# Kernel optimization log

Hardware: AMD Instinct MI355X
Metric: run time of the kernel (lower is better)

Reference implementation:

```python
import jax, jax.numpy as jnp
import numpy as np

N_HEAD = 8
EPS_LN = 1e-5
EPS_SM = 1e-16


def _mlp(x, w1, b1, g, beta, w2, b2):
    # Linear -> ReLU -> LayerNorm -> Linear (matches nn.Sequential in torch module)
    h = jax.nn.relu(x @ w1 + b1)
    mu = jnp.mean(h, axis=-1, keepdims=True)
    var = jnp.mean((h - mu) ** 2, axis=-1, keepdims=True)
    h = (h - mu) * jax.lax.rsqrt(var + EPS_LN) * g + beta
    return h @ w2 + b2


def setup_inputs() -> dict:
    B, L, D, E, Fe, H = 4, 4096, 128, 262144, 5, N_HEAD
    ks = jax.random.split(jax.random.key(0), 20)
    s = 0.02
    p = lambda i, sh: jax.random.normal(ks[i], sh, jnp.float32) * s
    z = lambda n: jnp.zeros((n,), jnp.float32)
    inp = {
        "key": jax.random.normal(ks[0], (B, L, D), jnp.float32),
        "value": jax.random.normal(ks[1], (B, L, D), jnp.float32),
        "query": jax.random.normal(ks[2], (B, L, D), jnp.float32),
        "edge_feats": jax.random.normal(ks[3], (E, Fe), jnp.float32),
        "atten_masks": jnp.zeros((E,), jnp.float32),  # present in signature, unused in forward
        "batch_indices": jax.random.randint(ks[4], (E,), 0, B),
        "head_indices": jax.random.randint(ks[5], (E,), 0, L),
        "tail_indices": jax.random.randint(ks[6], (E,), 0, L),
        "key_w": p(7, (D, D)), "key_b": z(D),
        "query_w": p(8, (D, D)), "query_b": z(D),
        "value_w": p(9, (D, D)), "value_b": z(D),
        "proj_w": p(10, (D, D)), "proj_b": z(D),
        "ea_w1": p(11, (Fe, D)), "ea_b1": z(D), "ea_g": jnp.ones((D,), jnp.float32), "ea_beta": z(D), "ea_w2": p(12, (D, H)), "ea_b2": z(H),
        "ek_w1": p(13, (Fe, D)), "ek_b1": z(D), "ek_g": jnp.ones((D,), jnp.float32), "ek_beta": z(D), "ek_w2": p(14, (D, D)), "ek_b2": z(D),
        "ev_w1": p(15, (Fe, D)), "ev_b1": z(D), "ev_g": jnp.ones((D,), jnp.float32), "ev_beta": z(D), "ev_w2": p(16, (D, D)), "ev_b2": z(D),
    }
    return inp


def reference(key, value, query, edge_feats, atten_masks,
              batch_indices, head_indices, tail_indices,
              key_w, key_b, query_w, query_b, value_w, value_b, proj_w, proj_b,
              ea_w1, ea_b1, ea_g, ea_beta, ea_w2, ea_b2,
              ek_w1, ek_b1, ek_g, ek_beta, ek_w2, ek_b2,
              ev_w1, ev_b1, ev_g, ev_beta, ev_w2, ev_b2):
    B, L, D = query.shape
    H = N_HEAD
    dh = D // H
    N = B * L
    # node projections -> [B*L, H, dh]
    k = (key @ key_w + key_b).reshape(N, H, dh)
    q = (query @ query_w + query_b).reshape(N, H, dh)
    v = (value @ value_w + value_b).reshape(N, H, dh)
    heads = batch_indices * L + head_indices  # destination node per edge
    tails = batch_indices * L + tail_indices  # source node per edge
    # per-edge gather + edge-conditioned k/v
    qs = q[heads]
    ks = k[tails] + _mlp(edge_feats, ek_w1, ek_b1, ek_g, ek_beta, ek_w2, ek_b2).reshape(-1, H, dh)
    vs = v[tails] + _mlp(edge_feats, ev_w1, ev_b1, ev_g, ev_beta, ev_w2, ev_b2).reshape(-1, H, dh)
    w = jnp.sum(ks * qs, axis=-1) + _mlp(edge_feats, ea_w1, ea_b1, ea_g, ea_beta, ea_w2, ea_b2)  # [E, H]
    # segment softmax over edges grouped by destination node
    m = jax.ops.segment_max(w, heads, num_segments=N)
    ex = jnp.exp(w - m[heads])
    denom = jax.ops.segment_sum(ex, heads, num_segments=N)
    att = ex / (denom[heads] + EPS_SM)  # [E, H]
    # weighted scatter-sum combine
    y = jax.ops.segment_sum(att[:, :, None] * vs, heads, num_segments=N).reshape(B, L, D)
    return y @ proj_w + proj_b
```

## Files before the change

kernel.cpp:

```cpp
#include <hip/hip_runtime.h>
#include <hip/hip_bf16.h>

#define D      128
#define NHEAD  8
#define FE     5
#define LSEQ   4096
#define EPB    64
#define NNODE  16384
#define EPS_LN 1e-5f
#define EPS_SM 1e-16f

typedef unsigned short ushort_t;
typedef __bf16 bf16x8 __attribute__((ext_vector_type(8)));
typedef float  f32x4  __attribute__((ext_vector_type(4)));

__device__ __forceinline__ ushort_t f2bf(float x) {
    __hip_bfloat16 b = __float2bfloat16(x);
    return __builtin_bit_cast(unsigned short, b);
}
__device__ __forceinline__ float bf2f(ushort_t u) {
    __hip_bfloat16 b = __builtin_bit_cast(__hip_bfloat16, u);
    return __bfloat162float(b);
}
__device__ __forceinline__ float i2f(int x)  { return __builtin_bit_cast(float, x); }
__device__ __forceinline__ int   f2i(float x){ return __builtin_bit_cast(int, x); }

union Pk8 { ushort_t u[8]; uint4 v; };

__global__ __launch_bounds__(256) void pre_kernel(
    const float* __restrict__ ekw2, const float* __restrict__ evw2,
    const float* __restrict__ eaw2,
    const float* __restrict__ kw, const float* __restrict__ qw,
    const float* __restrict__ vw,
    ushort_t* __restrict__ eksw, ushort_t* __restrict__ evsw, ushort_t* __restrict__ easw,
    ushort_t* __restrict__ kwsw, ushort_t* __restrict__ qwsw, ushort_t* __restrict__ vwsw,
    const int* __restrict__ bidx, const int* __restrict__ hidx,
    int* __restrict__ cnt, int E)
{
    const int t = threadIdx.x;
    if (blockIdx.x < 41) {
        const int g = blockIdx.x * 256 + t;
        const float* src; ushort_t* dst; int frag, ncols = 128, nvalid = 128;
        if (g < 2048)       { src = ekw2; dst = eksw; frag = g; }
        else if (g < 4096)  { src = evw2; dst = evsw; frag = g - 2048; }
        else if (g < 4352)  { src = eaw2; dst = easw; frag = g - 4096; ncols = 8; nvalid = 8; }
        else if (g < 6400)  { src = kw;   dst = kwsw; frag = g - 4352; }
        else if (g < 8448)  { src = qw;   dst = qwsw; frag = g - 6400; }
        else if (g < 10496) { src = vw;   dst = vwsw; frag = g - 8448; }
        else return;
        const int s = (frag >> 6) & 3;
        const int l = frag & 63;
        const int n = ((frag >> 8) << 4) + (l & 15);
        Pk8 pk;
        #pragma unroll
        for (int j = 0; j < 8; ++j) {
            const int k = s * 32 + (l >> 4) * 8 + j;
            const float v = (n < nvalid) ? src[k * ncols + n] : 0.f;
            pk.u[j] = f2bf(v);
        }
        *(uint4*)(dst + (size_t)frag * 8) = pk.v;
        return;
    }
    const int e = (blockIdx.x - 41) * 256 + t;
    if (e < E) atomicAdd(&cnt[bidx[e] * LSEQ + hidx[e]], 1);
}

__global__ __launch_bounds__(1024) void scan16k(
    const int* __restrict__ cnt, int* __restrict__ base)
{
    __shared__ int part[1024];
    const int t = threadIdx.x;
    int v[16], ex[16], s = 0;
    #pragma unroll
    for (int i = 0; i < 16; ++i) v[i] = cnt[t * 16 + i];
    #pragma unroll
    for (int i = 0; i < 16; ++i) { ex[i] = s; s += v[i]; }
    part[t] = s;
    __syncthreads();
    for (int off = 1; off < 1024; off <<= 1) {
        const int x = (t >= off) ? part[t - off] : 0;
        __syncthreads();
        part[t] += x;
        __syncthreads();
    }
    const int boff = (t > 0) ? part[t - 1] : 0;
    #pragma unroll
    for (int i = 0; i < 16; ++i) base[t * 16 + i] = boff + ex[i];
    if (t == 1023) base[NNODE] = boff + s;
}

__global__ __launch_bounds__(256) void mid_kernel(
    const float* __restrict__ key, const float* __restrict__ value,
    const float* __restrict__ query,
    const float* __restrict__ key_b, const float* __restrict__ value_b,
    const float* __restrict__ query_b,
    const ushort_t* __restrict__ kwsw, const ushort_t* __restrict__ vwsw,
    const ushort_t* __restrict__ qwsw,
    ushort_t* __restrict__ k16, ushort_t* __restrict__ v16, ushort_t* __restrict__ q16,
    const int* __restrict__ bidx, const int* __restrict__ hidx, const int* __restrict__ tidx,
    const float* __restrict__ edge_feats,
    const int* __restrict__ base, int* __restrict__ cnt, float* __restrict__ rec,
    int nqm, int E)
{
    const int t  = threadIdx.x;
    const int nq = 3 * nqm;
    if ((int)blockIdx.x < nq) {
        const int which = blockIdx.x / nqm;
        const int blk   = blockIdx.x % nqm;
        const float* X     = (which == 0) ? key   : (which == 1) ? value   : query;
        const float* bias  = (which == 0) ? key_b : (which == 1) ? value_b : query_b;
        const ushort_t* Ww = (which == 0) ? kwsw  : (which == 1) ? vwsw    : qwsw;
        ushort_t* Y        = (which == 0) ? k16   : (which == 1) ? v16     : q16;

        const int mt    = t >> 6;
        const int l     = t & 63;
        const int rbase = blk * 64 + mt * 16;
        const int colb  = l & 15;
        const int row0  = (l >> 4) * 4;
        const int arow  = rbase + colb;
        const int koff  = (l >> 4) * 8;

        bf16x8 afr[4];
        #pragma unroll
        for (int s = 0; s < 4; ++s) {
            const float4 x0 = *(const float4*)&X[(size_t)arow * D + s * 32 + koff];
            const float4 x1 = *(const float4*)&X[(size_t)arow * D + s * 32 + koff + 4];
            Pk8 p8;
            p8.u[0] = f2bf(x0.x); p8.u[1] = f2bf(x0.y);
            p8.u[2] = f2bf(x0.z); p8.u[3] = f2bf(x0.w);
            p8.u[4] = f2bf(x1.x); p8.u[5] = f2bf(x1.y);
            p8.u[6] = f2bf(x1.z); p8.u[7] = f2bf(x1.w);
            afr[s] = __builtin_bit_cast(bf16x8, p8.v);
        }
        #pragma unroll
        for (int nt = 0; nt < 8; ++nt) {
            f32x4 acc = {0.f, 0.f, 0.f, 0.f};
            #pragma unroll
            for (int s = 0; s < 4; ++s) {
                const bf16x8 bfr = *(const bf16x8*)(Ww + (size_t)((nt * 4 + s) * 64 + l) * 8);
                acc = __builtin_amdgcn_mfma_f32_16x16x32_bf16(afr[s], bfr, acc, 0, 0, 0);
            }
            const int col = nt * 16 + colb;
            const float b = bias[col];
            #pragma unroll
            for (int r = 0; r < 4; ++r)
                Y[(size_t)(rbase + row0 + r) * D + col] = f2bf(acc[r] + b);
        }
        return;
    }

    const int e = (blockIdx.x - nq) * 256 + t;
    if (e >= E) return;
    const int bb = bidx[e];
    const int nh = bb * LSEQ + hidx[e];
    const int nt = bb * LSEQ + tidx[e];
    const int slot = atomicSub(&cnt[nh], 1) - 1;
    const int p = base[nh] + slot;
    float ef[FE];
    #pragma unroll
    for (int f = 0; f < FE; ++f) ef[f] = edge_feats[(size_t)e * FE + f];
    *(float4*)&rec[(size_t)p * 8]     = float4{ef[0], ef[1], ef[2], ef[3]};
    *(float4*)&rec[(size_t)p * 8 + 4] = float4{ef[4], i2f(nh), i2f(nt), 0.f};
}

__global__ __launch_bounds__(256, 4) void edge_kernel(
    const float* __restrict__ rec,
    const float* __restrict__ ea_w1, const float* __restrict__ ea_b1,
    const float* __restrict__ ea_g,  const float* __restrict__ ea_be, const float* __restrict__ ea_b2,
    const float* __restrict__ ek_w1, const float* __restrict__ ek_b1,
    const float* __restrict__ ek_g,  const float* __restrict__ ek_be, const float* __restrict__ ek_b2,
    const float* __restrict__ ev_w1, const float* __restrict__ ev_b1,
    const float* __restrict__ ev_g,  const float* __restrict__ ev_be, const float* __restrict__ ev_b2,
    const ushort_t* __restrict__ easw, const ushort_t* __restrict__ eksw, const ushort_t* __restrict__ evsw,
    const ushort_t* __restrict__ k16, const ushort_t* __restrict__ q16, const ushort_t* __restrict__ v16,
    float* __restrict__ ex_ws, ushort_t* __restrict__ vs_ws)
{
    __shared__ float pw1[3][FE * D];
    __shared__ float pb1[3][D], pg[3][D], pbe[3][D];
    __shared__ float pb2k[D], pb2v[D], pb2a[NHEAD];
    __shared__ float ef_s[EPB][FE];
    __shared__ int   eh_s[EPB], et_s[EPB];

    const int t   = threadIdx.x;
    const int e0g = blockIdx.x * EPB;

    for (int i = t; i < FE * D; i += 256) { pw1[0][i] = ea_w1[i]; pw1[1][i] = ek_w1[i]; pw1[2][i] = ev_w1[i]; }
    if (t < D) {
        pb1[0][t] = ea_b1[t]; pb1[1][t] = ek_b1[t]; pb1[2][t] = ev_b1[t];
        pg [0][t] = ea_g [t]; pg [1][t] = ek_g [t]; pg [2][t] = ev_g [t];
        pbe[0][t] = ea_be[t]; pbe[1][t] = ek_be[t]; pbe[2][t] = ev_be[t];
        pb2k[t] = ek_b2[t];   pb2v[t] = ev_b2[t];
        if (t < NHEAD) pb2a[t] = ea_b2[t];
    }
    if (t < 128) {
        const int pl = t >> 1, half = t & 1;
        const float4 v = *(const float4*)&rec[((size_t)e0g + pl) * 8 + half * 4];
        if (half == 0) {
            ef_s[pl][0] = v.x; ef_s[pl][1] = v.y; ef_s[pl][2] = v.z; ef_s[pl][3] = v.w;
        } else {
            ef_s[pl][4] = v.x; eh_s[pl] = f2i(v.y); et_s[pl] = f2i(v.z);
        }
    }
    __syncthreads();

    const int mt   = t >> 6;
    const int l    = t & 63;
    const int qt   = l & 3;
    const int per  = l >> 2;
    const int row0 = (l >> 4) * 4;
    const int colb = l & 15;
    const int src  = 4 * colb + (l >> 4);
    const int bsrc = (l & 48);

    int tn[4], hnn[4];
    #pragma unroll
    for (int r = 0; r < 4; ++r) { tn[r] = et_s[mt*16 + row0 + r]; hnn[r] = eh_s[mt*16 + row0 + r]; }

    float efr[FE];
    #pragma unroll
    for (int f = 0; f < FE; ++f) efr[f] = ef_s[mt*16 + per][f];

    auto first_layer = [&](int m, uint4 pk[4]) {
        const float4* w1v = (const float4*)&pw1[m][0];
        const float4* b1v = (const float4*)&pb1[m][0];
        const float4* gv  = (const float4*)&pg[m][0];
        const float4* bev = (const float4*)&pbe[m][0];
        float4 hv[4][2];
        float s1 = 0.f, s2 = 0.f;
        #pragma unroll
        for (int s = 0; s < 4; ++s) {
            #pragma unroll
            for (int hc = 0; hc < 2; ++hc) {
                const int idx = s * 8 + qt * 2 + hc;
                float4 a = b1v[idx];
                #pragma unroll
                for (int f = 0; f < FE; ++f) {
                    const float sc = efr[f];
                    const float4 w = w1v[f * 32 + idx];
                    a.x = fmaf(sc, w.x, a.x); a.y = fmaf(sc, w.y, a.y);
                    a.z = fmaf(sc, w.z, a.z); a.w = fmaf(sc, w.w, a.w);
                }
                a.x = fmaxf(a.x, 0.f); a.y = fmaxf(a.y, 0.f);
                a.z = fmaxf(a.z, 0.f); a.w = fmaxf(a.w, 0.f);
                hv[s][hc] = a;
                s1 += a.x + a.y + a.z + a.w;
                s2 += a.x*a.x + a.y*a.y + a.z*a.z + a.w*a.w;
            }
        }
        s1 += __shfl_xor(s1, 1); s1 += __shfl_xor(s1, 2);
        s2 += __shfl_xor(s2, 1); s2 += __shfl_xor(s2, 2);
        const float mu = s1 * (1.f / 128.f);
        const float rs = rsqrtf(s2 * (1.f / 128.f) - mu * mu + EPS_LN);
        #pragma unroll
        for (int s = 0; s < 4; ++s) {
            const int idx = s * 8 + qt * 2;
            const float4 x0 = hv[s][0], x1 = hv[s][1];
            const float4 g0 = gv[idx], g1 = gv[idx + 1];
            const float4 b0 = bev[idx], b1 = bev[idx + 1];
            Pk8 p8;
            p8.u[0] = f2bf(fmaf((x0.x - mu) * rs, g0.x, b0.x));
            p8.u[1] = f2bf(fmaf((x0.y - mu) * rs, g0.y, b0.y));
            p8.u[2] = f2bf(fmaf((x0.z - mu) * rs, g0.z, b0.z));
            p8.u[3] = f2bf(fmaf((x0.w - mu) * rs, g0.w, b0.w));
            p8.u[4] = f2bf(fmaf((x1.x - mu) * rs, g1.x, b1.x));
            p8.u[5] = f2bf(fmaf((x1.y - mu) * rs, g1.y, b1.y));
            p8.u[6] = f2bf(fmaf((x1.z - mu) * rs, g1.z, b1.z));
            p8.u[7] = f2bf(fmaf((x1.w - mu) * rs, g1.w, b1.w));
            pk[s] = p8.v;
        }
    };

    auto gather_afr = [&](const uint4 pk[4], bf16x8 afr[4]) {
        #pragma unroll
        for (int s = 0; s < 4; ++s) {
            uint4 w;
            w.x = (unsigned)__shfl((int)pk[s].x, src);
            w.y = (unsigned)__shfl((int)pk[s].y, src);
            w.z = (unsigned)__shfl((int)pk[s].z, src);
            w.w = (unsigned)__shfl((int)pk[s].w, src);
            afr[s] = __builtin_bit_cast(bf16x8, w);
        }
    };

    uint4 pk[4];
    bf16x8 afr[4];

    float eaacc[4];
    first_layer(0, pk);
    gather_afr(pk, afr);
    {
        f32x4 acc = {0.f, 0.f, 0.f, 0.f};
        #pragma unroll
        for (int s = 0; s < 4; ++s) {
            const bf16x8 bfr = *(const bf16x8*)(easw + (size_t)(s * 64 + l) * 8);
            acc = __builtin_amdgcn_mfma_f32_16x16x32_bf16(afr[s], bfr, acc, 0, 0, 0);
        }
        #pragma unroll
        for (int r = 0; r < 4; ++r) eaacc[r] = acc[r];
    }

    first_layer(1, pk);
    gather_afr(pk, afr);
    #pragma unroll
    for (int nt = 0; nt < NHEAD; ++nt) {
        f32x4 acc = {0.f, 0.f, 0.f, 0.f};
        #pragma unroll
        for (int s = 0; s < 4; ++s) {
            const bf16x8 bfr = *(const bf16x8*)(eksw + (size_t)((nt * 4 + s) * 64 + l) * 8);
            acc = __builtin_amdgcn_mfma_f32_16x16x32_bf16(afr[s], bfr, acc, 0, 0, 0);
        }
        const int col = nt * 16 + colb;
        const float b2 = pb2k[col];
        const float ba = pb2a[nt];
        float pr[4];
        #pragma unroll
        for (int r = 0; r < 4; ++r)
            pr[r] = (acc[r] + b2 + bf2f(k16[(size_t)tn[r] * D + col]))
                    * bf2f(q16[(size_t)hnn[r] * D + col]);
        #pragma unroll
        for (int m = 1; m < 16; m <<= 1) {
            #pragma unroll
            for (int r = 0; r < 4; ++r) pr[r] += __shfl_xor(pr[r], m);
        }
        #pragma unroll
        for (int r = 0; r < 4; ++r) {
            const float ea = __shfl(eaacc[r], bsrc | nt);
            const float ex = __expf(pr[r] + ea + ba);
            if (colb == nt)
                ex_ws[(size_t)(e0g + mt*16 + row0 + r) * NHEAD + nt] = ex;
        }
    }

    first_layer(2, pk);
    gather_afr(pk, afr);
    #pragma unroll
    for (int nt = 0; nt < NHEAD; ++nt) {
        f32x4 acc = {0.f, 0.f, 0.f, 0.f};
        #pragma unroll
        for (int s = 0; s < 4; ++s) {
            const bf16x8 bfr = *(const bf16x8*)(evsw + (size_t)((nt * 4 + s) * 64 + l) * 8);
            acc = __builtin_amdgcn_mfma_f32_16x16x32_bf16(afr[s], bfr, acc, 0, 0, 0);
        }
        const int col = nt * 16 + colb;
        const float b2 = pb2v[col];
        #pragma unroll
        for (int r = 0; r < 4; ++r) {
            const float vs = acc[r] + b2 + bf2f(v16[(size_t)tn[r] * D + col]);
            vs_ws[(size_t)(e0g + mt*16 + row0 + r) * D + col] = f2bf(vs);
        }
    }
}

__global__ __launch_bounds__(512) void agg_out(
    const int* __restrict__ base,
    const float* __restrict__ ex_ws, const ushort_t* __restrict__ vs_ws,
    const float* __restrict__ W, const float* __restrict__ bias,
    float* __restrict__ out)
{
    __shared__ float xs[D][20];
    const int t  = threadIdx.x;
    const int rg = t >> 7;
    const int j  = t & 127;
    const int h  = j >> 4;
    const int n0 = blockIdx.x * 16;

    #pragma unroll
    for (int ni = 0; ni < 4; ++ni) {
        const int n  = n0 + rg * 4 + ni;
        const int s0 = base[n], s1 = base[n + 1];
        float acc = 0.f, den = 0.f;
        int p = s0;
        for (; p + 4 <= s1; p += 4) {
            float ex4[4], vs4[4];
            #pragma unroll
            for (int r = 0; r < 4; ++r) {
                ex4[r] = ex_ws[(size_t)(p + r) * NHEAD + h];
                vs4[r] = bf2f(vs_ws[(size_t)(p + r) * D + j]);
            }
            #pragma unroll
            for (int r = 0; r < 4; ++r) {
                den += ex4[r];
                acc = fmaf(ex4[r], vs4[r], acc);
            }
        }
        for (; p < s1; ++p) {
            const float ex = ex_ws[(size_t)p * NHEAD + h];
            den += ex;
            acc = fmaf(ex, bf2f(vs_ws[(size_t)p * D + j]), acc);
        }
        xs[j][rg * 4 + ni] = acc / (den + EPS_SM);
    }
    __syncthreads();

    float acc[4];
    const float b = bias[j];
    #pragma unroll
    for (int r = 0; r < 4; ++r) acc[r] = b;
    #pragma unroll 4
    for (int i = 0; i < D; ++i) {
        const float w = W[i * D + j];
        const float4 y4 = *(const float4*)&xs[i][rg * 4];
        acc[0] = fmaf(y4.x, w, acc[0]); acc[1] = fmaf(y4.y, w, acc[1]);
        acc[2] = fmaf(y4.z, w, acc[2]); acc[3] = fmaf(y4.w, w, acc[3]);
    }
    #pragma unroll
    for (int r = 0; r < 4; ++r)
        out[(size_t)(n0 + rg * 4 + r) * D + j] = acc[r];
}

extern "C" void kernel_launch(void* const* d_in, const int* in_sizes, int n_in,
                              void* d_out, int out_size, void* d_ws, size_t ws_size,
                              hipStream_t stream)
{
    const float* key        = (const float*)d_in[0];
    const float* value      = (const float*)d_in[1];
    const float* query      = (const float*)d_in[2];
    const float* edge_feats = (const float*)d_in[3];
    const int*   bidx       = (const int*)d_in[5];
    const int*   hidx       = (const int*)d_in[6];
    const int*   tidx       = (const int*)d_in[7];
    const float* key_w   = (const float*)d_in[8];  const float* key_b   = (const float*)d_in[9];
    const float* query_w = (const float*)d_in[10]; const float* query_b = (const float*)d_in[11];
    const float* value_w = (const float*)d_in[12]; const float* value_b = (const float*)d_in[13];
    const float* proj_w  = (const float*)d_in[14]; const float* proj_b  = (const float*)d_in[15];

    const int N = in_sizes[0] / D;
    const int E = in_sizes[5];

    char* ws = (char*)d_ws;
    ushort_t* k16   = (ushort_t*)ws; ws += (size_t)N * D * 2;
    ushort_t* q16   = (ushort_t*)ws; ws += (size_t)N * D * 2;
    ushort_t* v16   = (ushort_t*)ws; ws += (size_t)N * D * 2;
    float* ex_ws    = (float*)ws;    ws += (size_t)E * NHEAD * 4;
    ushort_t* vs_ws = (ushort_t*)ws; ws += (size_t)E * D * 2;
    float* rec      = (float*)ws;    ws += (size_t)E * 8 * 4;
    ushort_t* eksw  = (ushort_t*)ws; ws += (size_t)2048 * 8 * 2;
    ushort_t* evsw  = (ushort_t*)ws; ws += (size_t)2048 * 8 * 2;
    ushort_t* easw  = (ushort_t*)ws; ws += (size_t)256 * 8 * 2;
    ushort_t* kwsw  = (ushort_t*)ws; ws += (size_t)2048 * 8 * 2;
    ushort_t* qwsw  = (ushort_t*)ws; ws += (size_t)2048 * 8 * 2;
    ushort_t* vwsw  = (ushort_t*)ws; ws += (size_t)2048 * 8 * 2;
    int* base = (int*)ws;  ws += (size_t)(N + 1) * 4;
    int* cnt  = (int*)ws;  ws += (size_t)N * 4;

    const int nqm   = N / 64;
    const int nhist = (E + 255) / 256;

    hipMemsetAsync(cnt, 0, (size_t)N * 4, stream);

    pre_kernel<<<41 + nhist, 256, 0, stream>>>(
        (const float*)d_in[26], (const float*)d_in[32], (const float*)d_in[20],
        key_w, query_w, value_w,
        eksw, evsw, easw, kwsw, qwsw, vwsw,
        bidx, hidx, cnt, E);

    scan16k<<<1, 1024, 0, stream>>>(cnt, base);

    mid_kernel<<<3 * nqm + nhist, 256, 0, stream>>>(
        key, value, query,
        key_b, value_b, query_b,
        kwsw, vwsw, qwsw,
        k16, v16, q16,
        bidx, hidx, tidx, edge_feats,
        base, cnt, rec, nqm, E);

    edge_kernel<<<E / EPB, 256, 0, stream>>>(
        rec,
        (const float*)d_in[16], (const float*)d_in[17], (const float*)d_in[18],
        (const float*)d_in[19], (const float*)d_in[21],
        (const float*)d_in[22], (const float*)d_in[23], (const float*)d_in[24],
        (const float*)d_in[25], (const float*)d_in[27],
        (const float*)d_in[28], (const float*)d_in[29], (const float*)d_in[30],
        (const float*)d_in[31], (const float*)d_in[33],
        easw, eksw, evsw,
        k16, q16, v16,
        ex_ws, vs_ws);

    agg_out<<<N / 16, 512, 0, stream>>>(base, ex_ws, vs_ws, proj_w, proj_b, (float*)d_out);
}
```

Baseline: 293.5 us.

## Fuse softmax-weighted aggregation into edge kernel via atomic scatter into node accumulators

The edge kernel no longer writes per-edge exp weights and bf16 value rows to workspace. It accumulates exp sums and exp-weighted values directly into per-node float buffers with atomicAdd, first merging runs of consecutive edges that share a destination node (edges are sorted by destination). The aggregation kernel is replaced by a simpler out_gemm that divides numerator by denominator and applies the output projection over 16 rows per 128-thread block. This removes the E×D round trip through memory, at the cost of many global float atomics, non-deterministic summation order, and a larger memset.

Result: slower. 398.7 us (+35.8%).

```diff
diff --git a/kernel.cpp b/kernel.cpp
--- a/kernel.cpp
+++ b/kernel.cpp
@@ -173,7 +173,7 @@
     const float* __restrict__ ev_g,  const float* __restrict__ ev_be, const float* __restrict__ ev_b2,
     const ushort_t* __restrict__ easw, const ushort_t* __restrict__ eksw, const ushort_t* __restrict__ evsw,
     const ushort_t* __restrict__ k16, const ushort_t* __restrict__ q16, const ushort_t* __restrict__ v16,
-    float* __restrict__ ex_ws, ushort_t* __restrict__ vs_ws)
+    float* __restrict__ num_ws, float* __restrict__ den_ws)
 {
     __shared__ float pw1[3][FE * D];
     __shared__ float pb1[3][D], pg[3][D], pbe[3][D];
@@ -299,6 +299,7 @@
         for (int r = 0; r < 4; ++r) eaacc[r] = acc[r];
     }
 
+    float exsel[4] = {0.f, 0.f, 0.f, 0.f};
     first_layer(1, pk);
     gather_afr(pk, afr);
     #pragma unroll
@@ -326,9 +327,20 @@
         for (int r = 0; r < 4; ++r) {
             const float ea = __shfl(eaacc[r], bsrc | nt);
             const float ex = __expf(pr[r] + ea + ba);
-            if (colb == nt)
-                ex_ws[(size_t)(e0g + mt*16 + row0 + r) * NHEAD + nt] = ex;
-        }
+            if (colb == nt) exsel[r] = ex;
+        }
+    }
+    if (colb < NHEAD) {
+        float run = exsel[0]; int cur = hnn[0];
+        #pragma unroll
+        for (int r = 1; r < 4; ++r) {
+            if (hnn[r] == cur) run += exsel[r];
+            else {
+                atomicAdd(&den_ws[(size_t)cur * NHEAD + colb], run);
+                cur = hnn[r]; run = exsel[r];
+            }
+        }
+        atomicAdd(&den_ws[(size_t)cur * NHEAD + colb], run);
     }
 
     first_layer(2, pk);
@@ -343,69 +355,64 @@
         }
         const int col = nt * 16 + colb;
         const float b2 = pb2v[col];
+        float val[4];
         #pragma unroll
         for (int r = 0; r < 4; ++r) {
-            const float vs = acc[r] + b2 + bf2f(v16[(size_t)tn[r] * D + col]);
-            vs_ws[(size_t)(e0g + mt*16 + row0 + r) * D + col] = f2bf(vs);
-        }
-    }
-}
-
-__global__ __launch_bounds__(512) void agg_out(
-    const int* __restrict__ base,
-    const float* __restrict__ ex_ws, const ushort_t* __restrict__ vs_ws,
+            const float exb = __shfl(exsel[r], bsrc | nt);
+            const float vs  = acc[r] + b2 + bf2f(v16[(size_t)tn[r] * D + col]);
+            val[r] = exb * vs;
+        }
+        float run = val[0]; int cur = hnn[0];
+        #pragma unroll
+        for (int r = 1; r < 4; ++r) {
+            if (hnn[r] == cur) run += val[r];
+            else {
+                atomicAdd(&num_ws[(size_t)cur * D + col], run);
+                cur = hnn[r]; run = val[r];
+            }
+        }
+        atomicAdd(&num_ws[(size_t)cur * D + col], run);
+    }
+}
+
+__global__ __launch_bounds__(128) void out_gemm(
+    const float* __restrict__ num, const float* __restrict__ den,
     const float* __restrict__ W, const float* __restrict__ bias,
-    float* __restrict__ out)
+    float* __restrict__ Y)
 {
     __shared__ float xs[D][20];
-    const int t  = threadIdx.x;
-    const int rg = t >> 7;
-    const int j  = t & 127;
-    const int h  = j >> 4;
-    const int n0 = blockIdx.x * 16;
-
-    #pragma unroll
-    for (int ni = 0; ni < 4; ++ni) {
-        const int n  = n0 + rg * 4 + ni;
-        const int s0 = base[n], s1 = base[n + 1];
-        float acc = 0.f, den = 0.f;
-        int p = s0;
-        for (; p + 4 <= s1; p += 4) {
-            float ex4[4], vs4[4];
-            #pragma unroll
-            for (int r = 0; r < 4; ++r) {
-                ex4[r] = ex_ws[(size_t)(p + r) * NHEAD + h];
-                vs4[r] = bf2f(vs_ws[(size_t)(p + r) * D + j]);
-            }
-            #pragma unroll
-            for (int r = 0; r < 4; ++r) {
-                den += ex4[r];
-                acc = fmaf(ex4[r], vs4[r], acc);
-            }
-        }
-        for (; p < s1; ++p) {
-            const float ex = ex_ws[(size_t)p * NHEAD + h];
-            den += ex;
-            acc = fmaf(ex, bf2f(vs_ws[(size_t)p * D + j]), acc);
-        }
-        xs[j][rg * 4 + ni] = acc / (den + EPS_SM);
+    const int j  = threadIdx.x;
+    const int r0 = blockIdx.x * 16;
+    {
+        float tmp[16];
+        #pragma unroll
+        for (int r = 0; r < 16; ++r) {
+            const float d = den[(size_t)(r0 + r) * NHEAD + (j >> 4)];
+            tmp[r] = num[(size_t)(r0 + r) * D + j] / (d + EPS_SM);
+        }
+        #pragma unroll
+        for (int c = 0; c < 4; ++c)
+            *(float4*)&xs[j][c * 4] = float4{tmp[c*4], tmp[c*4+1], tmp[c*4+2], tmp[c*4+3]};
     }
     __syncthreads();
-
-    float acc[4];
+    float acc[16];
     const float b = bias[j];
     #pragma unroll
-    for (int r = 0; r < 4; ++r) acc[r] = b;
+    for (int r = 0; r < 16; ++r) acc[r] = b;
     #pragma unroll 4
     for (int i = 0; i < D; ++i) {
         const float w = W[i * D + j];
-        const float4 y4 = *(const float4*)&xs[i][rg * 4];
-        acc[0] = fmaf(y4.x, w, acc[0]); acc[1] = fmaf(y4.y, w, acc[1]);
-        acc[2] = fmaf(y4.z, w, acc[2]); acc[3] = fmaf(y4.w, w, acc[3]);
-    }
-    #pragma unroll
-    for (int r = 0; r < 4; ++r)
-        out[(size_t)(n0 + rg * 4 + r) * D + j] = acc[r];
+        #pragma unroll
+        for (int c = 0; c < 4; ++c) {
+            const float4 x4 = *(const float4*)&xs[i][c * 4];
+            acc[c*4+0] = fmaf(x4.x, w, acc[c*4+0]);
+            acc[c*4+1] = fmaf(x4.y, w, acc[c*4+1]);
+            acc[c*4+2] = fmaf(x4.z, w, acc[c*4+2]);
+            acc[c*4+3] = fmaf(x4.w, w, acc[c*4+3]);
+        }
+    }
+    #pragma unroll
+    for (int r = 0; r < 16; ++r) Y[(size_t)(r0 + r) * D + j] = acc[r];
 }
 
 extern "C" void kernel_launch(void* const* d_in, const int* in_sizes, int n_in,
@@ -431,8 +438,6 @@
     ushort_t* k16   = (ushort_t*)ws; ws += (size_t)N * D * 2;
     ushort_t* q16   = (ushort_t*)ws; ws += (size_t)N * D * 2;
     ushort_t* v16   = (ushort_t*)ws; ws += (size_t)N * D * 2;
-    float* ex_ws    = (float*)ws;    ws += (size_t)E * NHEAD * 4;
-    ushort_t* vs_ws = (ushort_t*)ws; ws += (size_t)E * D * 2;
     float* rec      = (float*)ws;    ws += (size_t)E * 8 * 4;
     ushort_t* eksw  = (ushort_t*)ws; ws += (size_t)2048 * 8 * 2;
     ushort_t* evsw  = (ushort_t*)ws; ws += (size_t)2048 * 8 * 2;
@@ -441,12 +446,14 @@
     ushort_t* qwsw  = (ushort_t*)ws; ws += (size_t)2048 * 8 * 2;
     ushort_t* vwsw  = (ushort_t*)ws; ws += (size_t)2048 * 8 * 2;
     int* base = (int*)ws;  ws += (size_t)(N + 1) * 4;
-    int* cnt  = (int*)ws;  ws += (size_t)N * 4;
+    int*   cnt    = (int*)ws;   ws += (size_t)N * 4;
+    float* den_ws = (float*)ws; ws += (size_t)N * NHEAD * 4;
+    float* num_ws = (float*)ws; ws += (size_t)N * D * 4;
 
     const int nqm   = N / 64;
     const int nhist = (E + 255) / 256;
 
-    hipMemsetAsync(cnt, 0, (size_t)N * 4, stream);
+    hipMemsetAsync(cnt, 0, (size_t)N * (4 + NHEAD * 4 + D * 4), stream);
 
     pre_kernel<<<41 + nhist, 256, 0, stream>>>(
         (const float*)d_in[26], (const float*)d_in[32], (const float*)d_in[20],
@@ -474,7 +481,7 @@
         (const float*)d_in[31], (const float*)d_in[33],
         easw, eksw, evsw,
         k16, q16, v16,
-        ex_ws, vs_ws);
-
-    agg_out<<<N / 16, 512, 0, stream>>>(base, ex_ws, vs_ws, proj_w, proj_b, (float*)d_out);
-}
+        num_ws, den_ws);
+
+    out_gemm<<<N / 16, 128, 0, stream>>>(num_ws, den_ws, proj_w, proj_b, (float*)d_out);
+}
```
